# Kernel optimization log

Hardware: AMD Instinct MI355X
Metric: run time of the kernel (lower is better)

Reference implementation:

```python
import jax, jax.numpy as jnp
import numpy as np

C = 512
M = 8            # n_heads
G = 32           # GroupNorm groups
EPS = 1e-6


def setup_inputs() -> dict:
    key = jax.random.key(0)
    ks = jax.random.split(key, 7)
    x = jax.random.normal(ks[0], (2, C, 64, 64), dtype=jnp.float32)
    gn_weight = jnp.ones((C,), jnp.float32)
    gn_bias = jnp.zeros((C,), jnp.float32)
    qkv_w = jax.random.normal(ks[1], (3 * C, C), jnp.float32) * (1.0 / np.sqrt(C))
    qkv_b = jnp.zeros((3 * C,), jnp.float32)
    # source zero-inits proj_out; we use small random weights so the attention
    proj_w = jax.random.normal(ks[2], (C, C), jnp.float32) * (0.02 / np.sqrt(C))
    proj_b = jnp.zeros((C,), jnp.float32)
    return {"x": x, "gn_weight": gn_weight, "gn_bias": gn_bias,
            "qkv_w": qkv_w, "qkv_b": qkv_b, "proj_w": proj_w, "proj_b": proj_b}


def _forward(x, gn_weight, gn_bias, qkv_w, qkv_b, proj_w, proj_b):
    b, c, H, W = x.shape
    n = H * W
    d = c // M
    xf = x.reshape(b, c, n)

    # GroupNorm(32, c, eps=1e-6, affine)
    xg = xf.reshape(b, G, (c // G) * n)
    mu = xg.mean(axis=-1, keepdims=True)
    var = xg.var(axis=-1, keepdims=True)
    xn = ((xg - mu) * jax.lax.rsqrt(var + EPS)).reshape(b, c, n)
    xn = xn * gn_weight[None, :, None] + gn_bias[None, :, None]

    # 1x1 conv -> qkv, then legacy reshape-then-split
    qkv = jnp.einsum('oc,bcn->bon', qkv_w, xn) + qkv_b[None, :, None]  # (b, 3c, n)
    qkv = qkv.reshape(b * M, 3 * d, n)
    q, k, v = qkv[:, :d], qkv[:, d:2 * d], qkv[:, 2 * d:]

    scale = 1.0 / np.sqrt(np.sqrt(d))
    w = jnp.einsum('Bdi,Bdj->Bij', q * scale, k * scale)  # (b*m, n, n)
    w = jax.nn.softmax(w, axis=-1)
    a = jnp.einsum('Bin,Bdn->Bdi', w, v)                  # (b*m, d, n)
    a = a.reshape(b, c, n)

    h = jnp.einsum('oc,bcn->bon', proj_w, a) + proj_b[None, :, None]
    # NOTE: source reassigns x = norm(x) before the residual add.
    return (xn + h).reshape(b, c, H, W)


def reference(x, gn_weight, gn_bias, qkv_w, qkv_b, proj_w, proj_b):
    return _forward(x, gn_weight, gn_bias, qkv_w, qkv_b, proj_w, proj_b)
```

## Files before the change

### kernel.cpp

```cpp
#include <hip/hip_runtime.h>
#include <cstdint>
#include <cstddef>

typedef __attribute__((ext_vector_type(8))) short short8;
typedef __attribute__((ext_vector_type(4))) float f32x4;

#define QSCALE 0.18033688011112043f

__device__ __forceinline__ float bf2f(unsigned short u) {
  return __uint_as_float(((unsigned)u) << 16);
}
__device__ __forceinline__ unsigned short f2bf(float f) {
  unsigned u = __float_as_uint(f);
  u += 0x7fffu + ((u >> 16) & 1u);
  return (unsigned short)(u >> 16);
}
__device__ __forceinline__ unsigned cvtpk(float a, float b) {
  unsigned r;
  asm("v_cvt_pk_bf16_f32 %0, %1, %2" : "=v"(r) : "v"(a), "v"(b));
  return r;
}
__device__ __forceinline__ short8 mk8(unsigned a, unsigned b, unsigned c, unsigned d) {
  union { unsigned u[4]; short8 s; } x;
  x.u[0] = a; x.u[1] = b; x.u[2] = c; x.u[3] = d;
  return x.s;
}
__device__ __forceinline__ void g2l16(const void* g, void* l) {
  __builtin_amdgcn_global_load_lds(
      (const __attribute__((address_space(1))) unsigned int*)g,
      (__attribute__((address_space(3))) unsigned int*)l, 16, 0, 0);
}

__global__ __launch_bounds__(256) void k_wgn(const float* __restrict__ wqf,
                                             const float* __restrict__ wpf,
                                             unsigned short* __restrict__ wq,
                                             unsigned short* __restrict__ wp,
                                             const float* __restrict__ x,
                                             float* __restrict__ part) {
  __shared__ float red[8];
  const int blk = blockIdx.x;
  const int t = threadIdx.x;
  if (blk < 1024) {
    int i = blk * 256 + t;
    if (i < 196608) {
      float4 v = ((const float4*)wqf)[i];
      ushort4 u;
      u.x = f2bf(v.x); u.y = f2bf(v.y); u.z = f2bf(v.z); u.w = f2bf(v.w);
      ((ushort4*)wq)[i] = u;
    } else {
      int k = i - 196608;
      float4 v = ((const float4*)wpf)[k];
      ushort4 u;
      u.x = f2bf(v.x); u.y = f2bf(v.y); u.z = f2bf(v.z); u.w = f2bf(v.w);
      ((ushort4*)wp)[k] = u;
    }
  } else {
    int b2 = blk - 1024;
    int bg = b2 >> 4, slice = b2 & 15;
    const float4* base = (const float4*)(x + (size_t)bg * 65536 + (size_t)slice * 4096);
    float s = 0.f, q = 0.f;
#pragma unroll
    for (int i = 0; i < 4; ++i) {
      float4 v = base[t + i * 256];
      s += v.x + v.y + v.z + v.w;
      q += v.x * v.x + v.y * v.y + v.z * v.z + v.w * v.w;
    }
#pragma unroll
    for (int off = 1; off < 64; off <<= 1) {
      s += __shfl_xor(s, off);
      q += __shfl_xor(q, off);
    }
    int wid = t >> 6;
    if ((t & 63) == 0) { red[wid * 2] = s; red[wid * 2 + 1] = q; }
    __syncthreads();
    if (t == 0) {
      float S = red[0] + red[2] + red[4] + red[6];
      float Q = red[1] + red[3] + red[5] + red[7];
      part[b2 * 2] = S;
      part[b2 * 2 + 1] = Q;
    }
  }
}

__global__ void k_gnfin(const float* __restrict__ part, float* __restrict__ stats) {
  int t = threadIdx.x;
  float S = 0.f, Q = 0.f;
#pragma unroll
  for (int i = 0; i < 16; ++i) {
    S += part[(t * 16 + i) * 2];
    Q += part[(t * 16 + i) * 2 + 1];
  }
  float mean = S * (1.f / 65536.f);
  float var = Q * (1.f / 65536.f) - mean * mean;
  stats[t * 2] = mean;
  stats[t * 2 + 1] = rsqrtf(var + 1e-6f);
}

__global__ __launch_bounds__(256) void k_gnnorm(const float* __restrict__ x,
                                                const float* __restrict__ gnw,
                                                const float* __restrict__ gnb,
                                                const float* __restrict__ stats,
                                                unsigned short* __restrict__ xn,
                                                unsigned short* __restrict__ xnT) {
  __shared__ float T[64 * 65];
  const int t = threadIdx.x;
  const int n0 = blockIdx.x * 64, c0 = blockIdx.y * 64, bb = blockIdx.z;
#pragma unroll
  for (int p = 0; p < 4; ++p) {
    int s = p * 256 + t;
    int row = s >> 4, seg = s & 15;
    int c = c0 + row;
    int gi = bb * 32 + (c >> 4);
    float mean = stats[gi * 2], rstd = stats[gi * 2 + 1];
    float gw = gnw[c] * rstd;
    float gb = gnb[c] - mean * gw;
    float4 v = *(const float4*)(x + ((size_t)bb * 512 + c) * 4096 + n0 + seg * 4);
    float f0 = v.x * gw + gb, f1 = v.y * gw + gb, f2 = v.z * gw + gb, f3 = v.w * gw + gb;
    ushort4 u;
    u.x = f2bf(f0); u.y = f2bf(f1); u.z = f2bf(f2); u.w = f2bf(f3);
    *(ushort4*)(xn + ((size_t)bb * 512 + c) * 4096 + n0 + seg * 4) = u;
    T[(seg * 4 + 0) * 65 + row] = f0;
    T[(seg * 4 + 1) * 65 + row] = f1;
    T[(seg * 4 + 2) * 65 + row] = f2;
    T[(seg * 4 + 3) * 65 + row] = f3;
  }
  __syncthreads();
#pragma unroll
  for (int p = 0; p < 4; ++p) {
    int s = p * 256 + t;
    int nl = s >> 4, cs = s & 15;
    float f0 = T[nl * 65 + cs * 4 + 0];
    float f1 = T[nl * 65 + cs * 4 + 1];
    float f2 = T[nl * 65 + cs * 4 + 2];
    float f3 = T[nl * 65 + cs * 4 + 3];
    ushort4 u;
    u.x = f2bf(f0); u.y = f2bf(f1); u.z = f2bf(f2); u.w = f2bf(f3);
    *(ushort4*)(xnT + ((size_t)bb * 4096 + n0 + nl) * 512 + c0 + cs * 4) = u;
  }
}

template <int MODE>
__global__ __launch_bounds__(256) void k_gemm(
    const unsigned short* __restrict__ A,
    const unsigned short* __restrict__ Bt,
    const float* __restrict__ bias,
    unsigned short* __restrict__ outA,
    unsigned short* __restrict__ outT,
    const unsigned short* __restrict__ resid,
    float* __restrict__ outF,
    int Mo) {
  __shared__ char lds[34816];
  const int t = threadIdx.x;
  const int lane = t & 63;
  const int g = lane >> 4, ln = lane & 15;
  const int wid = t >> 6, wr = wid >> 1, wc = wid & 1;
  const int bn0 = blockIdx.x * 128, bm0 = blockIdx.y * 128, bb = blockIdx.z;

  const unsigned short* Ab = A + (size_t)bm0 * 512;
  const unsigned short* Bb = Bt + ((size_t)bb * 4096 + bn0) * 512;

  f32x4 acc[4][4];
#pragma unroll
  for (int m = 0; m < 4; ++m)
#pragma unroll
    for (int n = 0; n < 4; ++n) acc[m][n] = f32x4{0.f, 0.f, 0.f, 0.f};

#pragma unroll 1
  for (int kt = 0; kt < 8; ++kt) {
#pragma unroll
    for (int p = 0; p < 4; ++p) {
      int s = p * 256 + t;
      int row = s >> 3;
      int csg = (s & 7) ^ (row & 7);
      g2l16(Ab + (size_t)row * 512 + kt * 64 + csg * 8,
            &lds[(p * 256 + (t & ~63)) * 16]);
    }
#pragma unroll
    for (int p = 0; p < 4; ++p) {
      int s = p * 256 + t;
      int row = s >> 3;
      int csg = (s & 7) ^ (row & 7);
      g2l16(Bb + (size_t)row * 512 + kt * 64 + csg * 8,
            &lds[16384 + (p * 256 + (t & ~63)) * 16]);
    }
    __syncthreads();
#pragma unroll
    for (int kk = 0; kk < 2; ++kk) {
      short8 af[4], bfr[4];
#pragma unroll
      for (int m = 0; m < 4; ++m) {
        int row = wr * 64 + m * 16 + ln;
        int cs = (kk * 4 + g) ^ (row & 7);
        af[m] = *(const short8*)&lds[row * 128 + cs * 16];
      }
#pragma unroll
      for (int n = 0; n < 4; ++n) {
        int row = wc * 64 + n * 16 + ln;
        int cs = (kk * 4 + g) ^ (row & 7);
        bfr[n] = *(const short8*)&lds[16384 + row * 128 + cs * 16];
      }
      __builtin_amdgcn_s_setprio(1);
#pragma unroll
      for (int m = 0; m < 4; ++m)
#pragma unroll
        for (int n = 0; n < 4; ++n)
          acc[m][n] = __builtin_amdgcn_mfma_f32_16x16x32_bf16(af[m], bfr[n], acc[m][n], 0, 0, 0);
      __builtin_amdgcn_s_setprio(0);
    }
    __syncthreads();
  }

  if (MODE == 0) {
#pragma unroll
    for (int m = 0; m < 4; ++m)
#pragma unroll
      for (int n = 0; n < 4; ++n)
#pragma unroll
        for (int r = 0; r < 4; ++r) {
          int ol = wr * 64 + m * 16 + g * 4 + r;
          int jl = wc * 64 + n * 16 + ln;
          int o = bm0 + ol, j = bn0 + jl;
          float v = acc[m][n][r] + bias[o];
          unsigned short bv = f2bf(v);
          if ((o % 192) >= 128) {
            int jp = (j & ~63) | (j & 32) | ((j & 0xC) << 1) | ((j & 16) >> 2) | (j & 3);
            outA[((size_t)bb * 1536 + o) * 4096 + jp] = bv;
          }
          *(unsigned short*)&lds[jl * 272 + ol * 2] = bv;
        }
    __syncthreads();
#pragma unroll
    for (int p = 0; p < 8; ++p) {
      int s = p * 256 + t;
      int jl = s >> 4, cs = s & 15;
      int oo = bm0 + cs * 8;
      if ((oo % 192) < 128) {
        short8 v = *(const short8*)&lds[jl * 272 + cs * 16];
        *(short8*)&outT[((size_t)bb * 4096 + bn0 + jl) * 1536 + oo] = v;
      }
    }
  } else {
#pragma unroll
    for (int m = 0; m < 4; ++m)
#pragma unroll
      for (int n = 0; n < 4; ++n)
#pragma unroll
        for (int r = 0; r < 4; ++r) {
          int o = bm0 + wr * 64 + m * 16 + g * 4 + r;
          int j = bn0 + wc * 64 + n * 16 + ln;
          size_t idx = ((size_t)bb * 512 + o) * 4096 + j;
          outF[idx] = acc[m][n][r] + bias[o] + bf2f(resid[idx]);
        }
  }
}

__global__ __launch_bounds__(512, 4) void k_attn(const unsigned short* __restrict__ qkv,
                                                 const unsigned short* __restrict__ qkvT,
                                                 unsigned short* __restrict__ aT) {
  __shared__ char lds[49152];
  const int t = threadIdx.x, lane = t & 63;
  const int g = lane >> 4, ln = lane & 15;
  const int wid = t >> 6;
  const int h = blockIdx.y, bb = blockIdx.z;
  const int q0 = blockIdx.x * 128 + wid * 16;

  int kaddr[2][4], vaddr[2][4];
#pragma unroll
  for (int kk = 0; kk < 2; ++kk)
#pragma unroll
    for (int f = 0; f < 4; ++f) {
      int row = f * 16 + ln;
      int off = row * 128 + (((kk * 4 + g) ^ (row & 7)) << 4);
      kaddr[kk][f] = off;
      vaddr[kk][f] = 24576 + off;
    }

  const unsigned short* kS;
  const unsigned short* vS;
  int ldst;
  {
    int row = t >> 3, csg = (t & 7) ^ (row & 7);
    kS = qkvT + ((size_t)bb * 4096 + row) * 1536 + 192 * h + 64 + csg * 8;
    vS = qkv + ((size_t)bb * 1536 + 192 * h + 128 + row) * 4096 + csg * 8;
    ldst = (t & ~63) * 16;
  }

  short8 qf[2];
#pragma unroll
  for (int kk = 0; kk < 2; ++kk) {
    short8 v = *(const short8*)(qkvT + ((size_t)bb * 4096 + q0 + ln) * 1536 +
                                192 * h + kk * 32 + g * 8);
#pragma unroll
    for (int e = 0; e < 8; ++e) {
      float f = bf2f((unsigned short)v[e]) * QSCALE;
      v[e] = (short)f2bf(f);
    }
    qf[kk] = v;
  }

  const short8 onesb = mk8(0x3F803F80u, 0x3F803F80u, 0x3F803F80u, 0x3F803F80u);

  f32x4 acc[4];
  f32x4 lacc = f32x4{0.f, 0.f, 0.f, 0.f};
#pragma unroll
  for (int df = 0; df < 4; ++df) acc[df] = f32x4{0.f, 0.f, 0.f, 0.f};

  short8 pf[2];
  short8 vfp[2][4];

#pragma unroll
  for (int jt = 0; jt < 2; ++jt) {
    g2l16(kS, &lds[jt * 8192 + ldst]);
    g2l16(vS, &lds[24576 + jt * 8192 + ldst]);
    kS += 64 * 1536;
    vS += 64;
  }

  {
    asm volatile("s_waitcnt vmcnt(2)" ::: "memory");
    __builtin_amdgcn_s_barrier();
    __builtin_amdgcn_sched_barrier(0);
    g2l16(kS, &lds[2 * 8192 + ldst]);
    g2l16(vS, &lds[24576 + 2 * 8192 + ldst]);
    kS += 64 * 1536;
    vS += 64;
    const char* Kc = &lds[0];
    short8 kf[2][4];
#pragma unroll
    for (int kk = 0; kk < 2; ++kk)
#pragma unroll
      for (int f = 0; f < 4; ++f) kf[kk][f] = *(const short8*)(Kc + kaddr[kk][f]);
    const f32x4 zf = f32x4{0.f, 0.f, 0.f, 0.f};
    f32x4 w[4];
    __builtin_amdgcn_s_setprio(1);
#pragma unroll
    for (int jf = 0; jf < 4; ++jf)
      w[jf] = __builtin_amdgcn_mfma_f32_16x16x32_bf16(kf[0][jf], qf[0], zf, 0, 0, 0);
#pragma unroll
    for (int jf = 0; jf < 4; ++jf)
      w[jf] = __builtin_amdgcn_mfma_f32_16x16x32_bf16(kf[1][jf], qf[1], w[jf], 0, 0, 0);
    __builtin_amdgcn_s_setprio(0);
#pragma unroll
    for (int jf = 0; jf < 4; ++jf)
#pragma unroll
      for (int r = 0; r < 4; ++r) w[jf][r] = __builtin_amdgcn_exp2f(w[jf][r]);
#pragma unroll
    for (int kk = 0; kk < 2; ++kk)
      pf[kk] = mk8(cvtpk(w[2 * kk][0], w[2 * kk][1]),
                   cvtpk(w[2 * kk][2], w[2 * kk][3]),
                   cvtpk(w[2 * kk + 1][0], w[2 * kk + 1][1]),
                   cvtpk(w[2 * kk + 1][2], w[2 * kk + 1][3]));
#pragma unroll
    for (int kk = 0; kk < 2; ++kk)
#pragma unroll
      for (int f = 0; f < 4; ++f) vfp[kk][f] = *(const short8*)(Kc + vaddr[kk][f]);
  }

#pragma unroll 3
  for (int jt = 1; jt < 64; ++jt) {
    const int cur = jt % 3;
    const char* Kc = &lds[cur * 8192];
    if (jt < 63) {
      asm volatile("s_waitcnt vmcnt(2) lgkmcnt(0)" ::: "memory");
    } else {
      asm volatile("s_waitcnt vmcnt(0) lgkmcnt(0)" ::: "memory");
    }
    __builtin_amdgcn_s_barrier();
    __builtin_amdgcn_sched_barrier(0);

    if (jt < 62) {
      int nb = (jt + 2) % 3;
      g2l16(kS, &lds[nb * 8192 + ldst]);
      g2l16(vS, &lds[24576 + nb * 8192 + ldst]);
      kS += 64 * 1536;
      vS += 64;
    }

    short8 kf[2][4];
#pragma unroll
    for (int kk = 0; kk < 2; ++kk)
#pragma unroll
      for (int f = 0; f < 4; ++f) kf[kk][f] = *(const short8*)(Kc + kaddr[kk][f]);

    const f32x4 zf = f32x4{0.f, 0.f, 0.f, 0.f};
    f32x4 w[4];
    __builtin_amdgcn_s_setprio(1);
#pragma unroll
    for (int jf = 0; jf < 4; ++jf)
      w[jf] = __builtin_amdgcn_mfma_f32_16x16x32_bf16(kf[0][jf], qf[0], zf, 0, 0, 0);
#pragma unroll
    for (int jf = 0; jf < 4; ++jf)
      w[jf] = __builtin_amdgcn_mfma_f32_16x16x32_bf16(kf[1][jf], qf[1], w[jf], 0, 0, 0);
    __builtin_amdgcn_sched_barrier(0);

#pragma unroll
    for (int jf = 0; jf < 4; ++jf)
#pragma unroll
      for (int r = 0; r < 4; ++r) w[jf][r] = __builtin_amdgcn_exp2f(w[jf][r]);
    short8 npf[2];
#pragma unroll
    for (int kk = 0; kk < 2; ++kk)
      npf[kk] = mk8(cvtpk(w[2 * kk][0], w[2 * kk][1]),
                    cvtpk(w[2 * kk][2], w[2 * kk][3]),
                    cvtpk(w[2 * kk + 1][0], w[2 * kk + 1][1]),
                    cvtpk(w[2 * kk + 1][2], w[2 * kk + 1][3]));
#pragma unroll
    for (int kk = 0; kk < 2; ++kk) {
#pragma unroll
      for (int df = 0; df < 4; ++df)
        acc[df] = __builtin_amdgcn_mfma_f32_16x16x32_bf16(pf[kk], vfp[kk][df], acc[df], 0, 0, 0);
      lacc = __builtin_amdgcn_mfma_f32_16x16x32_bf16(pf[kk], onesb, lacc, 0, 0, 0);
    }
#pragma unroll
    for (int i = 0; i < 10; ++i) {
      __builtin_amdgcn_sched_group_barrier(0x8, 1, 0);
      __builtin_amdgcn_sched_group_barrier(0x2, 2, 0);
    }
    __builtin_amdgcn_sched_barrier(0);
    __builtin_amdgcn_s_setprio(0);

    pf[0] = npf[0];
    pf[1] = npf[1];
#pragma unroll
    for (int kk = 0; kk < 2; ++kk)
#pragma unroll
      for (int f = 0; f < 4; ++f) vfp[kk][f] = *(const short8*)(Kc + vaddr[kk][f]);
  }

  __builtin_amdgcn_s_setprio(1);
#pragma unroll
  for (int kk = 0; kk < 2; ++kk) {
#pragma unroll
    for (int df = 0; df < 4; ++df)
      acc[df] = __builtin_amdgcn_mfma_f32_16x16x32_bf16(pf[kk], vfp[kk][df], acc[df], 0, 0, 0);
    lacc = __builtin_amdgcn_mfma_f32_16x16x32_bf16(pf[kk], onesb, lacc, 0, 0, 0);
  }
  __builtin_amdgcn_s_setprio(0);

#pragma unroll
  for (int r = 0; r < 4; ++r) {
    float inv = 1.f / lacc[r];
    int row = q0 + g * 4 + r;
#pragma unroll
    for (int df = 0; df < 4; ++df)
      aT[((size_t)bb * 4096 + row) * 512 + h * 64 + df * 16 + ln] =
          f2bf(acc[df][r] * inv);
  }
}

extern "C" void kernel_launch(void* const* d_in, const int* in_sizes, int n_in,
                              void* d_out, int out_size, void* d_ws, size_t ws_size,
                              hipStream_t stream) {
  const float* x     = (const float*)d_in[0];
  const float* gnw   = (const float*)d_in[1];
  const float* gnb   = (const float*)d_in[2];
  const float* qkvw  = (const float*)d_in[3];
  const float* qkvb  = (const float*)d_in[4];
  const float* projw = (const float*)d_in[5];
  const float* projb = (const float*)d_in[6];
  float* out = (float*)d_out;
  char* ws = (char*)d_ws;

  const size_t OFF_WQ   = 0;
  const size_t OFF_WP   = 1572864;
  const size_t OFF_XN   = 2097152;
  const size_t OFF_XNT  = 10485760;
  const size_t OFF_QKV  = 18874368;
  const size_t OFF_QKVT = 44040192;
  const size_t OFF_AT   = 69206016;
  const size_t OFF_PART = 77594624;
  const size_t OFF_STAT = 77602816;

  unsigned short* wq   = (unsigned short*)(ws + OFF_WQ);
  unsigned short* wp   = (unsigned short*)(ws + OFF_WP);
  unsigned short* xn   = (unsigned short*)(ws + OFF_XN);
  unsigned short* xnT  = (unsigned short*)(ws + OFF_XNT);
  unsigned short* qkv  = (unsigned short*)(ws + OFF_QKV);
  unsigned short* qkvT = (unsigned short*)(ws + OFF_QKVT);
  unsigned short* aT   = (unsigned short*)(ws + OFF_AT);
  float* part  = (float*)(ws + OFF_PART);
  float* stats = (float*)(ws + OFF_STAT);

  k_wgn<<<dim3(2048), dim3(256), 0, stream>>>(qkvw, projw, wq, wp, x, part);
  k_gnfin<<<dim3(1), dim3(64), 0, stream>>>(part, stats);
  k_gnnorm<<<dim3(64, 8, 2), dim3(256), 0, stream>>>(x, gnw, gnb, stats, xn, xnT);
  k_gemm<0><<<dim3(32, 12, 2), dim3(256), 0, stream>>>(wq, xnT, qkvb, qkv, qkvT, nullptr, nullptr, 1536);
  k_attn<<<dim3(32, 8, 2), dim3(512), 0, stream>>>(qkv, qkvT, aT);
  k_gemm<1><<<dim3(32, 4, 2), dim3(256), 0, stream>>>(wp, aT, projb, nullptr, nullptr, xn, out, 512);
}
```

Measured before the change: 130.4 us.

## Stagger QK and PV phase order across wave halves in attention loop

Splits the eight waves into two groups by a wave-uniform parity bit. One group runs QK^T, exp and then PV each iteration; the other runs PV first, then QK^T and exp. The aim is to keep the matrix units busy while the other group is doing exp work, in a ping-pong style. In exchange it drops the explicit sched_group_barrier interleaving and duplicates the loop body, which adds code size and may change register pressure.

New measurement: 164.2 us. 1.26x slower.

```diff
diff --git a/kernel.cpp b/kernel.cpp
--- a/kernel.cpp
+++ b/kernel.cpp
@@ -261,6 +261,7 @@
   const int t = threadIdx.x, lane = t & 63;
   const int g = lane >> 4, ln = lane & 15;
   const int wid = t >> 6;
+  const int wpar = __builtin_amdgcn_readfirstlane(wid >> 2) & 1;
   const int h = blockIdx.y, bb = blockIdx.z;
   const int q0 = blockIdx.x * 128 + wid * 16;
 
@@ -376,48 +377,78 @@
       vS += 64;
     }
 
-    short8 kf[2][4];
-#pragma unroll
-    for (int kk = 0; kk < 2; ++kk)
-#pragma unroll
-      for (int f = 0; f < 4; ++f) kf[kk][f] = *(const short8*)(Kc + kaddr[kk][f]);
-
     const f32x4 zf = f32x4{0.f, 0.f, 0.f, 0.f};
-    f32x4 w[4];
-    __builtin_amdgcn_s_setprio(1);
-#pragma unroll
-    for (int jf = 0; jf < 4; ++jf)
-      w[jf] = __builtin_amdgcn_mfma_f32_16x16x32_bf16(kf[0][jf], qf[0], zf, 0, 0, 0);
-#pragma unroll
-    for (int jf = 0; jf < 4; ++jf)
-      w[jf] = __builtin_amdgcn_mfma_f32_16x16x32_bf16(kf[1][jf], qf[1], w[jf], 0, 0, 0);
-    __builtin_amdgcn_sched_barrier(0);
-
-#pragma unroll
-    for (int jf = 0; jf < 4; ++jf)
-#pragma unroll
-      for (int r = 0; r < 4; ++r) w[jf][r] = __builtin_amdgcn_exp2f(w[jf][r]);
     short8 npf[2];
-#pragma unroll
-    for (int kk = 0; kk < 2; ++kk)
-      npf[kk] = mk8(cvtpk(w[2 * kk][0], w[2 * kk][1]),
-                    cvtpk(w[2 * kk][2], w[2 * kk][3]),
-                    cvtpk(w[2 * kk + 1][0], w[2 * kk + 1][1]),
-                    cvtpk(w[2 * kk + 1][2], w[2 * kk + 1][3]));
-#pragma unroll
-    for (int kk = 0; kk < 2; ++kk) {
-#pragma unroll
-      for (int df = 0; df < 4; ++df)
-        acc[df] = __builtin_amdgcn_mfma_f32_16x16x32_bf16(pf[kk], vfp[kk][df], acc[df], 0, 0, 0);
-      lacc = __builtin_amdgcn_mfma_f32_16x16x32_bf16(pf[kk], onesb, lacc, 0, 0, 0);
-    }
-#pragma unroll
-    for (int i = 0; i < 10; ++i) {
-      __builtin_amdgcn_sched_group_barrier(0x8, 1, 0);
-      __builtin_amdgcn_sched_group_barrier(0x2, 2, 0);
-    }
-    __builtin_amdgcn_sched_barrier(0);
-    __builtin_amdgcn_s_setprio(0);
+
+    if (wpar == 0) {
+      short8 kf[2][4];
+#pragma unroll
+      for (int kk = 0; kk < 2; ++kk)
+#pragma unroll
+        for (int f = 0; f < 4; ++f) kf[kk][f] = *(const short8*)(Kc + kaddr[kk][f]);
+      f32x4 w[4];
+      __builtin_amdgcn_s_setprio(1);
+#pragma unroll
+      for (int jf = 0; jf < 4; ++jf)
+        w[jf] = __builtin_amdgcn_mfma_f32_16x16x32_bf16(kf[0][jf], qf[0], zf, 0, 0, 0);
+#pragma unroll
+      for (int jf = 0; jf < 4; ++jf)
+        w[jf] = __builtin_amdgcn_mfma_f32_16x16x32_bf16(kf[1][jf], qf[1], w[jf], 0, 0, 0);
+      __builtin_amdgcn_s_setprio(0);
+#pragma unroll
+      for (int jf = 0; jf < 4; ++jf)
+#pragma unroll
+        for (int r = 0; r < 4; ++r) w[jf][r] = __builtin_amdgcn_exp2f(w[jf][r]);
+#pragma unroll
+      for (int kk = 0; kk < 2; ++kk)
+        npf[kk] = mk8(cvtpk(w[2 * kk][0], w[2 * kk][1]),
+                      cvtpk(w[2 * kk][2], w[2 * kk][3]),
+                      cvtpk(w[2 * kk + 1][0], w[2 * kk + 1][1]),
+                      cvtpk(w[2 * kk + 1][2], w[2 * kk + 1][3]));
+      __builtin_amdgcn_s_setprio(1);
+#pragma unroll
+      for (int kk = 0; kk < 2; ++kk) {
+#pragma unroll
+        for (int df = 0; df < 4; ++df)
+          acc[df] = __builtin_amdgcn_mfma_f32_16x16x32_bf16(pf[kk], vfp[kk][df], acc[df], 0, 0, 0);
+        lacc = __builtin_amdgcn_mfma_f32_16x16x32_bf16(pf[kk], onesb, lacc, 0, 0, 0);
+      }
+      __builtin_amdgcn_s_setprio(0);
+    } else {
+      __builtin_amdgcn_s_setprio(1);
+#pragma unroll
+      for (int kk = 0; kk < 2; ++kk) {
+#pragma unroll
+        for (int df = 0; df < 4; ++df)
+          acc[df] = __builtin_amdgcn_mfma_f32_16x16x32_bf16(pf[kk], vfp[kk][df], acc[df], 0, 0, 0);
+        lacc = __builtin_amdgcn_mfma_f32_16x16x32_bf16(pf[kk], onesb, lacc, 0, 0, 0);
+      }
+      __builtin_amdgcn_s_setprio(0);
+      short8 kf[2][4];
+#pragma unroll
+      for (int kk = 0; kk < 2; ++kk)
+#pragma unroll
+        for (int f = 0; f < 4; ++f) kf[kk][f] = *(const short8*)(Kc + kaddr[kk][f]);
+      f32x4 w[4];
+      __builtin_amdgcn_s_setprio(1);
+#pragma unroll
+      for (int jf = 0; jf < 4; ++jf)
+        w[jf] = __builtin_amdgcn_mfma_f32_16x16x32_bf16(kf[0][jf], qf[0], zf, 0, 0, 0);
+#pragma unroll
+      for (int jf = 0; jf < 4; ++jf)
+        w[jf] = __builtin_amdgcn_mfma_f32_16x16x32_bf16(kf[1][jf], qf[1], w[jf], 0, 0, 0);
+      __builtin_amdgcn_s_setprio(0);
+#pragma unroll
+      for (int jf = 0; jf < 4; ++jf)
+#pragma unroll
+        for (int r = 0; r < 4; ++r) w[jf][r] = __builtin_amdgcn_exp2f(w[jf][r]);
+#pragma unroll
+      for (int kk = 0; kk < 2; ++kk)
+        npf[kk] = mk8(cvtpk(w[2 * kk][0], w[2 * kk][1]),
+                      cvtpk(w[2 * kk][2], w[2 * kk][3]),
+                      cvtpk(w[2 * kk + 1][0], w[2 * kk + 1][1]),
+                      cvtpk(w[2 * kk + 1][2], w[2 * kk + 1][3]));
+    }
 
     pf[0] = npf[0];
     pf[1] = npf[1];
```

## Split attention key tiles across wave pairs and reduce partial outputs in LDS

Applied to the files above, without the earlier changes.

Each pair of waves now shares 32 query rows and splits every 64-key tile in half, so each wave loads half as many K fragments and reuses each K and V fragment across two query sub-tiles. Partial numerators and denominators are then summed through LDS before normalising and writing. The software pipelining that overlapped the P·V MFMAs of one tile with the QK and exp2 work of the next is removed, which makes the loop simpler but exposes more latency. The change also adds an end-of-kernel LDS reduction, two barriers, and more accumulator registers per wave.

Result: faster. 125.5 us (-3.8%).

```diff
diff --git a/kernel.cpp b/kernel.cpp
--- a/kernel.cpp
+++ b/kernel.cpp
@@ -261,19 +261,24 @@
   const int t = threadIdx.x, lane = t & 63;
   const int g = lane >> 4, ln = lane & 15;
   const int wid = t >> 6;
+  const int qw = wid >> 1;
+  const int jw = wid & 1;
   const int h = blockIdx.y, bb = blockIdx.z;
-  const int q0 = blockIdx.x * 128 + wid * 16;
-
-  int kaddr[2][4], vaddr[2][4];
+  const int q0 = blockIdx.x * 128 + qw * 32;
+
+  int kaddr[2][2], vaddr[4];
 #pragma unroll
   for (int kk = 0; kk < 2; ++kk)
 #pragma unroll
-    for (int f = 0; f < 4; ++f) {
-      int row = f * 16 + ln;
-      int off = row * 128 + (((kk * 4 + g) ^ (row & 7)) << 4);
-      kaddr[kk][f] = off;
-      vaddr[kk][f] = 24576 + off;
-    }
+    for (int jf = 0; jf < 2; ++jf) {
+      int row = jw * 32 + jf * 16 + ln;
+      kaddr[kk][jf] = row * 128 + (((kk * 4 + g) ^ (row & 7)) << 4);
+    }
+#pragma unroll
+  for (int df = 0; df < 4; ++df) {
+    int row = df * 16 + ln;
+    vaddr[df] = 24576 + row * 128 + (((jw * 4 + g) ^ (row & 7)) << 4);
+  }
 
   const unsigned short* kS;
   const unsigned short* vS;
@@ -285,28 +290,31 @@
     ldst = (t & ~63) * 16;
   }
 
-  short8 qf[2];
-#pragma unroll
-  for (int kk = 0; kk < 2; ++kk) {
-    short8 v = *(const short8*)(qkvT + ((size_t)bb * 4096 + q0 + ln) * 1536 +
-                                192 * h + kk * 32 + g * 8);
-#pragma unroll
-    for (int e = 0; e < 8; ++e) {
-      float f = bf2f((unsigned short)v[e]) * QSCALE;
-      v[e] = (short)f2bf(f);
-    }
-    qf[kk] = v;
-  }
+  short8 qf[2][2];
+#pragma unroll
+  for (int qt = 0; qt < 2; ++qt)
+#pragma unroll
+    for (int kk = 0; kk < 2; ++kk) {
+      short8 v = *(const short8*)(qkvT + ((size_t)bb * 4096 + q0 + qt * 16 + ln) * 1536 +
+                                  192 * h + kk * 32 + g * 8);
+#pragma unroll
+      for (int e = 0; e < 8; ++e) {
+        float f = bf2f((unsigned short)v[e]) * QSCALE;
+        v[e] = (short)f2bf(f);
+      }
+      qf[qt][kk] = v;
+    }
 
   const short8 onesb = mk8(0x3F803F80u, 0x3F803F80u, 0x3F803F80u, 0x3F803F80u);
 
-  f32x4 acc[4];
-  f32x4 lacc = f32x4{0.f, 0.f, 0.f, 0.f};
-#pragma unroll
-  for (int df = 0; df < 4; ++df) acc[df] = f32x4{0.f, 0.f, 0.f, 0.f};
-
-  short8 pf[2];
-  short8 vfp[2][4];
+  f32x4 acc[2][4];
+  f32x4 lacc[2];
+#pragma unroll
+  for (int qt = 0; qt < 2; ++qt) {
+#pragma unroll
+    for (int df = 0; df < 4; ++df) acc[qt][df] = f32x4{0.f, 0.f, 0.f, 0.f};
+    lacc[qt] = f32x4{0.f, 0.f, 0.f, 0.f};
+  }
 
 #pragma unroll
   for (int jt = 0; jt < 2; ++jt) {
@@ -316,48 +324,8 @@
     vS += 64;
   }
 
-  {
-    asm volatile("s_waitcnt vmcnt(2)" ::: "memory");
-    __builtin_amdgcn_s_barrier();
-    __builtin_amdgcn_sched_barrier(0);
-    g2l16(kS, &lds[2 * 8192 + ldst]);
-    g2l16(vS, &lds[24576 + 2 * 8192 + ldst]);
-    kS += 64 * 1536;
-    vS += 64;
-    const char* Kc = &lds[0];
-    short8 kf[2][4];
-#pragma unroll
-    for (int kk = 0; kk < 2; ++kk)
-#pragma unroll
-      for (int f = 0; f < 4; ++f) kf[kk][f] = *(const short8*)(Kc + kaddr[kk][f]);
-    const f32x4 zf = f32x4{0.f, 0.f, 0.f, 0.f};
-    f32x4 w[4];
-    __builtin_amdgcn_s_setprio(1);
-#pragma unroll
-    for (int jf = 0; jf < 4; ++jf)
-      w[jf] = __builtin_amdgcn_mfma_f32_16x16x32_bf16(kf[0][jf], qf[0], zf, 0, 0, 0);
-#pragma unroll
-    for (int jf = 0; jf < 4; ++jf)
-      w[jf] = __builtin_amdgcn_mfma_f32_16x16x32_bf16(kf[1][jf], qf[1], w[jf], 0, 0, 0);
-    __builtin_amdgcn_s_setprio(0);
-#pragma unroll
-    for (int jf = 0; jf < 4; ++jf)
-#pragma unroll
-      for (int r = 0; r < 4; ++r) w[jf][r] = __builtin_amdgcn_exp2f(w[jf][r]);
-#pragma unroll
-    for (int kk = 0; kk < 2; ++kk)
-      pf[kk] = mk8(cvtpk(w[2 * kk][0], w[2 * kk][1]),
-                   cvtpk(w[2 * kk][2], w[2 * kk][3]),
-                   cvtpk(w[2 * kk + 1][0], w[2 * kk + 1][1]),
-                   cvtpk(w[2 * kk + 1][2], w[2 * kk + 1][3]));
-#pragma unroll
-    for (int kk = 0; kk < 2; ++kk)
-#pragma unroll
-      for (int f = 0; f < 4; ++f) vfp[kk][f] = *(const short8*)(Kc + vaddr[kk][f]);
-  }
-
 #pragma unroll 3
-  for (int jt = 1; jt < 64; ++jt) {
+  for (int jt = 0; jt < 64; ++jt) {
     const int cur = jt % 3;
     const char* Kc = &lds[cur * 8192];
     if (jt < 63) {
@@ -376,75 +344,89 @@
       vS += 64;
     }
 
-    short8 kf[2][4];
+    short8 kf[2][2];
 #pragma unroll
     for (int kk = 0; kk < 2; ++kk)
 #pragma unroll
-      for (int f = 0; f < 4; ++f) kf[kk][f] = *(const short8*)(Kc + kaddr[kk][f]);
+      for (int jf = 0; jf < 2; ++jf) kf[kk][jf] = *(const short8*)(Kc + kaddr[kk][jf]);
 
     const f32x4 zf = f32x4{0.f, 0.f, 0.f, 0.f};
-    f32x4 w[4];
+    f32x4 w[2][2];
     __builtin_amdgcn_s_setprio(1);
 #pragma unroll
-    for (int jf = 0; jf < 4; ++jf)
-      w[jf] = __builtin_amdgcn_mfma_f32_16x16x32_bf16(kf[0][jf], qf[0], zf, 0, 0, 0);
-#pragma unroll
-    for (int jf = 0; jf < 4; ++jf)
-      w[jf] = __builtin_amdgcn_mfma_f32_16x16x32_bf16(kf[1][jf], qf[1], w[jf], 0, 0, 0);
-    __builtin_amdgcn_sched_barrier(0);
-
-#pragma unroll
-    for (int jf = 0; jf < 4; ++jf)
-#pragma unroll
-      for (int r = 0; r < 4; ++r) w[jf][r] = __builtin_amdgcn_exp2f(w[jf][r]);
-    short8 npf[2];
-#pragma unroll
-    for (int kk = 0; kk < 2; ++kk)
-      npf[kk] = mk8(cvtpk(w[2 * kk][0], w[2 * kk][1]),
-                    cvtpk(w[2 * kk][2], w[2 * kk][3]),
-                    cvtpk(w[2 * kk + 1][0], w[2 * kk + 1][1]),
-                    cvtpk(w[2 * kk + 1][2], w[2 * kk + 1][3]));
-#pragma unroll
-    for (int kk = 0; kk < 2; ++kk) {
+    for (int qt = 0; qt < 2; ++qt)
+#pragma unroll
+      for (int jf = 0; jf < 2; ++jf)
+        w[qt][jf] = __builtin_amdgcn_mfma_f32_16x16x32_bf16(kf[0][jf], qf[qt][0], zf, 0, 0, 0);
+#pragma unroll
+    for (int qt = 0; qt < 2; ++qt)
+#pragma unroll
+      for (int jf = 0; jf < 2; ++jf)
+        w[qt][jf] = __builtin_amdgcn_mfma_f32_16x16x32_bf16(kf[1][jf], qf[qt][1], w[qt][jf], 0, 0, 0);
+    __builtin_amdgcn_s_setprio(0);
+
+    short8 vf[4];
+#pragma unroll
+    for (int df = 0; df < 4; ++df) vf[df] = *(const short8*)(Kc + vaddr[df]);
+
+#pragma unroll
+    for (int qt = 0; qt < 2; ++qt)
+#pragma unroll
+      for (int jf = 0; jf < 2; ++jf)
+#pragma unroll
+        for (int r = 0; r < 4; ++r) w[qt][jf][r] = __builtin_amdgcn_exp2f(w[qt][jf][r]);
+
+    short8 pf[2];
+#pragma unroll
+    for (int qt = 0; qt < 2; ++qt)
+      pf[qt] = mk8(cvtpk(w[qt][0][0], w[qt][0][1]),
+                   cvtpk(w[qt][0][2], w[qt][0][3]),
+                   cvtpk(w[qt][1][0], w[qt][1][1]),
+                   cvtpk(w[qt][1][2], w[qt][1][3]));
+
+    __builtin_amdgcn_s_setprio(1);
+#pragma unroll
+    for (int qt = 0; qt < 2; ++qt) {
 #pragma unroll
       for (int df = 0; df < 4; ++df)
-        acc[df] = __builtin_amdgcn_mfma_f32_16x16x32_bf16(pf[kk], vfp[kk][df], acc[df], 0, 0, 0);
-      lacc = __builtin_amdgcn_mfma_f32_16x16x32_bf16(pf[kk], onesb, lacc, 0, 0, 0);
-    }
-#pragma unroll
-    for (int i = 0; i < 10; ++i) {
-      __builtin_amdgcn_sched_group_barrier(0x8, 1, 0);
-      __builtin_amdgcn_sched_group_barrier(0x2, 2, 0);
-    }
-    __builtin_amdgcn_sched_barrier(0);
+        acc[qt][df] = __builtin_amdgcn_mfma_f32_16x16x32_bf16(pf[qt], vf[df], acc[qt][df], 0, 0, 0);
+      lacc[qt] = __builtin_amdgcn_mfma_f32_16x16x32_bf16(pf[qt], onesb, lacc[qt], 0, 0, 0);
+    }
     __builtin_amdgcn_s_setprio(0);
-
-    pf[0] = npf[0];
-    pf[1] = npf[1];
-#pragma unroll
-    for (int kk = 0; kk < 2; ++kk)
-#pragma unroll
-      for (int f = 0; f < 4; ++f) vfp[kk][f] = *(const short8*)(Kc + vaddr[kk][f]);
-  }
-
-  __builtin_amdgcn_s_setprio(1);
-#pragma unroll
-  for (int kk = 0; kk < 2; ++kk) {
-#pragma unroll
-    for (int df = 0; df < 4; ++df)
-      acc[df] = __builtin_amdgcn_mfma_f32_16x16x32_bf16(pf[kk], vfp[kk][df], acc[df], 0, 0, 0);
-    lacc = __builtin_amdgcn_mfma_f32_16x16x32_bf16(pf[kk], onesb, lacc, 0, 0, 0);
-  }
-  __builtin_amdgcn_s_setprio(0);
-
-#pragma unroll
-  for (int r = 0; r < 4; ++r) {
-    float inv = 1.f / lacc[r];
-    int row = q0 + g * 4 + r;
-#pragma unroll
-    for (int df = 0; df < 4; ++df)
-      aT[((size_t)bb * 4096 + row) * 512 + h * 64 + df * 16 + ln] =
-          f2bf(acc[df][r] * inv);
+  }
+
+  __syncthreads();
+  float* cb = (float*)lds;
+  const int cbase = qw * 2560;
+  if (jw == 1) {
+#pragma unroll
+    for (int qt = 0; qt < 2; ++qt) {
+#pragma unroll
+      for (int df = 0; df < 4; ++df)
+        *(f32x4*)&cb[cbase + ((qt * 4 + df) * 64 + lane) * 4] = acc[qt][df];
+      *(f32x4*)&cb[cbase + 2048 + (qt * 64 + lane) * 4] = lacc[qt];
+    }
+  }
+  __syncthreads();
+  if (jw == 0) {
+#pragma unroll
+    for (int qt = 0; qt < 2; ++qt) {
+#pragma unroll
+      for (int df = 0; df < 4; ++df)
+        acc[qt][df] += *(const f32x4*)&cb[cbase + ((qt * 4 + df) * 64 + lane) * 4];
+      lacc[qt] += *(const f32x4*)&cb[cbase + 2048 + (qt * 64 + lane) * 4];
+    }
+#pragma unroll
+    for (int qt = 0; qt < 2; ++qt)
+#pragma unroll
+      for (int r = 0; r < 4; ++r) {
+        float inv = 1.f / lacc[qt][r];
+        int row = q0 + qt * 16 + g * 4 + r;
+#pragma unroll
+        for (int df = 0; df < 4; ++df)
+          aT[((size_t)bb * 4096 + row) * 512 + h * 64 + df * 16 + ln] =
+              f2bf(acc[qt][df][r] * inv);
+      }
   }
 }
 
```
